# Kernel optimization log

Hardware: AMD Instinct MI355X
Metric: run time of the kernel (lower is better)

The kernel has to match this reference:

```python
import jax, jax.numpy as jnp
import numpy as np

N = 131072
IN_A = 256
IN_V = 512
IN_VF = 512
CH = 256
BN_EPS = 1e-5
COS_EPS = 1e-8


def setup_inputs() -> dict:
    key = jax.random.key(0)
    ks = jax.random.split(key, 12)
    s = 0.05
    return {
        "x": jax.random.normal(ks[0], (N, 4, 512), dtype=jnp.float32),
        "audio_node_mask": jax.random.bernoulli(ks[1], 0.5, (N,)),
        "W_a": jax.random.normal(ks[2], (IN_A, CH), dtype=jnp.float32) * s,
        "b_a": jnp.zeros((CH,), jnp.float32),
        "W_v": jax.random.normal(ks[3], (IN_V, CH), dtype=jnp.float32) * s,
        "b_v": jnp.zeros((CH,), jnp.float32),
        "W_f": jax.random.normal(ks[4], (2 * CH, CH), dtype=jnp.float32) * s,
        "b_f": jnp.zeros((CH,), jnp.float32),
        "gamma": jnp.ones((CH,), jnp.float32),
        "beta": jnp.zeros((CH,), jnp.float32),
        "W_fc": jax.random.normal(ks[5], (CH, 2), dtype=jnp.float32) * s,
        "b_fc": jnp.zeros((2,), jnp.float32),
    }


def reference(x, audio_node_mask, W_a, b_a, W_v, b_v, W_f, b_f, gamma, beta, W_fc, b_fc):
    # Slice per-type features (x: [N, 4, 512])
    a_in = x[:, 0, :IN_A]    # audio feats (also video->audio feats)
    v_in = x[:, 1, :IN_V]    # video feats
    a_vf = x[:, 2, :IN_VF]   # audio voice-face emb
    v_vf = x[:, 3, :IN_VF]   # video voice-face emb

    # cosine similarity along feature dim (torch.nn.functional.cosine_similarity semantics)
    dot = jnp.sum(a_vf * v_vf, axis=1)
    denom = jnp.maximum(jnp.linalg.norm(a_vf, axis=1) * jnp.linalg.norm(v_vf, axis=1), COS_EPS)
    sim = dot / denom  # [N]

    # per-type linears (compute densely, select by mask -> same math as masked scatter)
    a_out = a_in @ W_a + b_a                                   # [N, CH]
    v_out = v_in @ W_v + b_v                                   # [N, CH]
    va = a_in * sim[:, None]                                   # sim-weighted audio feats on video nodes
    fused = jnp.concatenate([va, v_out], axis=1) @ W_f + b_f   # [N, CH]

    graph_feats = jnp.where(audio_node_mask[:, None], a_out, fused)

    # BatchNorm1d (training: batch statistics, biased variance)
    mu = jnp.mean(graph_feats, axis=0)
    var = jnp.mean(jnp.square(graph_feats - mu), axis=0)
    graph_feats = (graph_feats - mu) * jax.lax.rsqrt(var + BN_EPS) * gamma + beta

    graph_feats = jax.nn.relu(graph_feats)
    return graph_feats @ W_fc + b_fc  # [N, 2]
```

## Files before the change

kernel.cpp:

```cpp
#include <hip/hip_runtime.h>
#include <hip/hip_bf16.h>
#include <stdint.h>

#define NN 131072
#define NB2 2050

typedef unsigned int uint;
typedef unsigned short ushort;
typedef __attribute__((ext_vector_type(8))) __bf16 bf16x8;
typedef __attribute__((ext_vector_type(2))) __bf16 bf16x2;
typedef __attribute__((ext_vector_type(4))) float f32x4;


__device__ __forceinline__ ushort f2bf(float f) {
    uint u = __float_as_uint(f);
    u += 0x7FFF + ((u >> 16) & 1);
    return (ushort)(u >> 16);
}
__device__ __forceinline__ uint pk2(float a, float b) {
    bf16x2 t;
    t[0] = (__bf16)a;
    t[1] = (__bf16)b;
    return __builtin_bit_cast(uint, t);
}
__device__ __forceinline__ bool mask_val(const unsigned char* m8, int flag, int i) {
    return flag ? (m8[(size_t)i * 4] != 0) : (m8[i] != 0);
}
__device__ __forceinline__ size_t pack_off(int k, int c) {
    return (size_t)(((k >> 5) * 16 + (c >> 4)) * 512
                    + (((k >> 3) & 3) * 16 + (c & 15)) * 8 + (k & 7));
}

__global__ void k_detect(const uint4* m128, int n, int* cntNZ) {
    __shared__ int cnt;
    if (threadIdx.x == 0) cnt = 0;
    __syncthreads();
    int local = 0;
    int nv = n >> 4;
    #pragma unroll 4
    for (int i = threadIdx.x; i < nv; i += 1024) {
        uint4 v = m128[i];
        if ((v.x | v.y | v.z | v.w) & 0x0000FF00u) local = 1;
    }
    if (local) atomicAdd(&cnt, 1);
    __syncthreads();
    if (threadIdx.x == 0) *cntNZ = cnt;
}

__global__ void k_count(const unsigned char* m8, const int* cntNZp, int* cntM) {
    int flag = (*cntNZp == 0) ? 1 : 0;
    int t = threadIdx.x;
    bool m = mask_val(m8, flag, blockIdx.x * 256 + t);
    unsigned long long bal = __ballot(m);
    __shared__ int wsum[4];
    if ((t & 63) == 0) wsum[t >> 6] = __popcll(bal);
    __syncthreads();
    if (t == 0) cntM[blockIdx.x] = wsum[0] + wsum[1] + wsum[2] + wsum[3];
}

__global__ void k_scan(const int* __restrict__ cntM, int* __restrict__ meta,
                       int* __restrict__ baseA, int* __restrict__ baseF) {
    __shared__ int sA[512], sF[512];
    int t = threadIdx.x;
    int a = cntM[t], f = 256 - a;
    sA[t] = a; sF[t] = f;
    __syncthreads();
    for (int off = 1; off < 512; off <<= 1) {
        int va = (t >= off) ? sA[t - off] : 0;
        int vf = (t >= off) ? sF[t - off] : 0;
        __syncthreads();
        sA[t] += va; sF[t] += vf;
        __syncthreads();
    }
    baseA[t] = sA[t] - a;
    baseF[t] = sF[t] - f;
    if (t == 511) { meta[2] = sA[511]; meta[1] = sF[511]; }
}

__global__ void k_fill(const unsigned char* m8, const int* cntNZp,
                       const int* __restrict__ baseA, const int* __restrict__ baseF,
                       int* __restrict__ audioIdx, int* __restrict__ fusedIdx) {
    int flag = (*cntNZp == 0) ? 1 : 0;
    int blk = blockIdx.x, t = threadIdx.x;
    int row = blk * 256 + t;
    bool m = mask_val(m8, flag, row);
    unsigned long long bal = __ballot(m);
    int lane = t & 63, w = t >> 6;
    unsigned long long lt = (1ull << lane) - 1ull;
    int pA = __popcll(bal & lt);
    __shared__ int wA[4];
    if (lane == 0) wA[w] = __popcll(bal);
    __syncthreads();
    int offA = 0;
    for (int i = 0; i < w; ++i) offA += wA[i];
    int offF = w * 64 - offA;
    int pF = lane - pA;
    if (m) audioIdx[baseA[blk] + offA + pA] = row;
    else   fusedIdx[baseF[blk] + offF + pF] = row;
}

__global__ void k_prep(const float* __restrict__ Wa, const float* __restrict__ Wf,
                       const float* __restrict__ Wv, const float* __restrict__ bv,
                       const float* __restrict__ bf_, ushort* __restrict__ Bwa,
                       ushort* __restrict__ Bwf, float* __restrict__ cf) {
    int c = threadIdx.x;
    int b = blockIdx.x;
    if (b < 256) {
        Bwa[pack_off(b, c)] = f2bf(Wa[b * 256 + c]);
    } else if (b < 512) {
        Bwf[pack_off(512 + (b - 256), c)] = f2bf(Wf[(b - 256) * 256 + c]);
    } else if (b < 1024) {
        int k = b - 512;
        const float* wr = Wv + k * 256;
        float acc = 0.f;
        #pragma unroll 8
        for (int j = 0; j < 256; ++j) acc += wr[j] * Wf[(256 + j) * 256 + c];
        Bwf[pack_off(k, c)] = f2bf(acc);
    } else {
        float acc = bf_[c];
        #pragma unroll 8
        for (int j = 0; j < 256; ++j) acc += bv[j] * Wf[(256 + j) * 256 + c];
        cf[c] = acc;
    }
}

__global__ __launch_bounds__(512, 4) void k_main(
    const float* __restrict__ x, const int* __restrict__ meta,
    const int* __restrict__ fusedIdx, const int* __restrict__ audioIdx,
    const ushort* __restrict__ Bwa, const ushort* __restrict__ Bwf,
    const float* __restrict__ ba, const float* __restrict__ cf,
    ushort* __restrict__ gf, float* __restrict__ bn_s, float* __restrict__ bn_q)
{
    __shared__ ushort As[2][64 * 256];
    __shared__ int ridxS[64];
    __shared__ float simS[64];
    __shared__ unsigned char validS[64];
    __shared__ float redS[256], redQ[256];

    const int tid = threadIdx.x;
    const int cntF = meta[1], cntA = meta[2];
    const int nbF = (cntF + 63) >> 6;
    const int nbA = (cntA + 63) >> 6;
    const int b = blockIdx.x;
    const bool isF = b < nbF;
    const int bb = isF ? b : b - nbF;

    if (!isF && bb >= nbA) {
        if (tid < 256) {
            bn_s[(size_t)b * 256 + tid] = 0.f;
            bn_q[(size_t)b * 256 + tid] = 0.f;
        }
        return;
    }

    const int cnt = isF ? cntF : cntA;
    const int* idxArr = isF ? fusedIdx : audioIdx;
    const int lane = tid & 63;
    const int w = tid >> 6, wr = w >> 2, wc = w & 3;
    const int fr = lane & 15, fg = lane >> 4;

    if (tid < 64) {
        int gpos = bb * 64 + tid;
        int ok = gpos < cnt;
        ridxS[tid] = ok ? idxArr[gpos] : 0;
        validS[tid] = ok;
        simS[tid] = 1.f;
    }
    if (tid < 256) { redS[tid] = 0.f; redQ[tid] = 0.f; }
    __syncthreads();

    const int sr2 = tid >> 3, kq = tid & 7;
    const float* xrow = x + (size_t)ridxS[sr2] * 2048;
    const float sVf = validS[sr2] ? 1.f : 0.f;

    f32x4 t0_, t1_, t2_, t3_, t4_, t5_, t6_, t7_;
    auto loadV = [&](int baseF_) {
        const f32x4* src = (const f32x4*)(xrow + baseF_) + kq * 8;
        t0_ = src[0]; t1_ = src[1]; t2_ = src[2]; t3_ = src[3];
        t4_ = src[4]; t5_ = src[5]; t6_ = src[6]; t7_ = src[7];
    };
    auto storeV = [&](int buf, float scl) {
        ushort* dst = As[buf] + sr2 * 256;
        int sx = sr2 & 7;
        uint4 q;
        q.x = pk2(t0_.x * scl, t0_.y * scl); q.y = pk2(t0_.z * scl, t0_.w * scl);
        q.z = pk2(t1_.x * scl, t1_.y * scl); q.w = pk2(t1_.z * scl, t1_.w * scl);
        *(uint4*)(dst + (((kq * 4 + 0) ^ sx) << 3)) = q;
        q.x = pk2(t2_.x * scl, t2_.y * scl); q.y = pk2(t2_.z * scl, t2_.w * scl);
        q.z = pk2(t3_.x * scl, t3_.y * scl); q.w = pk2(t3_.z * scl, t3_.w * scl);
        *(uint4*)(dst + (((kq * 4 + 1) ^ sx) << 3)) = q;
        q.x = pk2(t4_.x * scl, t4_.y * scl); q.y = pk2(t4_.z * scl, t4_.w * scl);
        q.z = pk2(t5_.x * scl, t5_.y * scl); q.w = pk2(t5_.z * scl, t5_.w * scl);
        *(uint4*)(dst + (((kq * 4 + 2) ^ sx) << 3)) = q;
        q.x = pk2(t6_.x * scl, t6_.y * scl); q.y = pk2(t6_.z * scl, t6_.w * scl);
        q.z = pk2(t7_.x * scl, t7_.y * scl); q.w = pk2(t7_.z * scl, t7_.w * scl);
        *(uint4*)(dst + (((kq * 4 + 3) ^ sx) << 3)) = q;
    };

    const ushort* bBase = (isF ? Bwf : Bwa) + ((size_t)(wc * 4) << 9) + (lane << 3);
    const int r0 = wr * 32 + fr, r1 = r0 + 16;
    const ushort* prd0 = As[0] + r0 * 256;
    const int sx0 = r0 & 7, sx1 = r1 & 7;

    f32x4 acc[2][4];
    #pragma unroll
    for (int m = 0; m < 2; ++m)
        #pragma unroll
        for (int n = 0; n < 4; ++n) acc[m][n] = (f32x4){0.f, 0.f, 0.f, 0.f};

    auto compute4 = [&](int buf, int visit) {
        const ushort* p0 = As[buf] + r0 * 256;
        const ushort* p1 = As[buf] + r1 * 256;
        #pragma unroll
        for (int st = 0; st < 4; ++st) {
            #pragma unroll
            for (int kk = 0; kk < 2; ++kk) {
                int sl = st * 8 + kk * 4 + fg;
                bf16x8 a0 = *(const bf16x8*)(p0 + ((sl ^ sx0) << 3));
                bf16x8 a1 = *(const bf16x8*)(p1 + ((sl ^ sx1) << 3));
                int kb = (visit * 4 + st) * 2 + kk;
                #pragma unroll
                for (int n = 0; n < 4; ++n) {
                    bf16x8 bv = *(const bf16x8*)(bBase + ((size_t)(kb * 16 + n) << 9));
                    acc[0][n] = __builtin_amdgcn_mfma_f32_16x16x32_bf16(a0, bv, acc[0][n], 0, 0, 0);
                    acc[1][n] = __builtin_amdgcn_mfma_f32_16x16x32_bf16(a1, bv, acc[1][n], 0, 0, 0);
                }
            }
        }
    };

    if (isF) {
        loadV(512);
        #pragma unroll 2
        for (int rr = 0; rr < 8; ++rr) {
            int r = w * 8 + rr;
            const f32x4* p = (const f32x4*)(x + (size_t)ridxS[r] * 2048 + 1024);
            f32x4 a0 = p[lane], a1 = p[lane + 64];
            f32x4 v0 = p[lane + 128], v1 = p[lane + 192];
            float dot = a0.x * v0.x + a0.y * v0.y + a0.z * v0.z + a0.w * v0.w
                      + a1.x * v1.x + a1.y * v1.y + a1.z * v1.z + a1.w * v1.w;
            float na = a0.x * a0.x + a0.y * a0.y + a0.z * a0.z + a0.w * a0.w
                     + a1.x * a1.x + a1.y * a1.y + a1.z * a1.z + a1.w * a1.w;
            float nv = v0.x * v0.x + v0.y * v0.y + v0.z * v0.z + v0.w * v0.w
                     + v1.x * v1.x + v1.y * v1.y + v1.z * v1.z + v1.w * v1.w;
            #pragma unroll
            for (int off = 32; off; off >>= 1) {
                dot += __shfl_xor(dot, off);
                na  += __shfl_xor(na,  off);
                nv  += __shfl_xor(nv,  off);
            }
            if (lane == 0)
                simS[r] = dot / fmaxf(sqrtf(na * nv), 1e-8f);
        }
        storeV(0, sVf);
        loadV(768);
        __syncthreads();
        compute4(0, 0);
        storeV(1, sVf);
        float sAf = validS[sr2] ? simS[sr2] : 0.f;
        __syncthreads();
        loadV(0);
        compute4(1, 1);
        storeV(0, sAf);
        __syncthreads();
        compute4(0, 2);
    } else {
        loadV(0);
        storeV(0, sVf);
        __syncthreads();
        compute4(0, 0);
    }

    const int colLo = wc * 64 + fr;
    const float* biasp = isF ? cf : ba;
    float bN[4];
    #pragma unroll
    for (int n = 0; n < 4; ++n) bN[n] = biasp[colLo + n * 16];

    float cs[4] = {0.f, 0.f, 0.f, 0.f}, cq[4] = {0.f, 0.f, 0.f, 0.f};
    #pragma unroll
    for (int m = 0; m < 2; ++m) {
        #pragma unroll
        for (int j = 0; j < 4; ++j) {
            int rloc = wr * 32 + m * 16 + fg * 4 + j;
            if (validS[rloc]) {
                ushort* grow = gf + (size_t)ridxS[rloc] * 256;
                #pragma unroll
                for (int n = 0; n < 4; ++n) {
                    float g = acc[m][n][j] + bN[n];
                    grow[colLo + n * 16] = f2bf(g);
                    cs[n] += g;
                    cq[n] += g * g;
                }
            }
        }
    }
    #pragma unroll
    for (int n = 0; n < 4; ++n) {
        atomicAdd(&redS[colLo + n * 16], cs[n]);
        atomicAdd(&redQ[colLo + n * 16], cq[n]);
    }
    __syncthreads();
    if (tid < 256) {
        bn_s[(size_t)b * 256 + tid] = redS[tid];
        bn_q[(size_t)b * 256 + tid] = redQ[tid];
    }
}

__global__ void k_stats(const float* __restrict__ bn_s, const float* __restrict__ bn_q,
                        const float* __restrict__ gamma, const float* __restrict__ beta,
                        float* __restrict__ scale, float* __restrict__ shift) {
    int c = blockIdx.x;
    int t = threadIdx.x;
    float s = 0.f, q = 0.f;
    for (int r = t; r < NB2; r += 256) {
        s += bn_s[(size_t)r * 256 + c];
        q += bn_q[(size_t)r * 256 + c];
    }
    __shared__ float ss[256], qq[256];
    ss[t] = s; qq[t] = q;
    __syncthreads();
    for (int off = 128; off; off >>= 1) {
        if (t < off) { ss[t] += ss[t + off]; qq[t] += qq[t + off]; }
        __syncthreads();
    }
    if (t == 0) {
        float mu  = ss[0] / 131072.f;
        float var = qq[0] / 131072.f - mu * mu;
        float sc = gamma[c] * rsqrtf(var + 1e-5f);
        scale[c] = sc;
        shift[c] = beta[c] - mu * sc;
    }
}

__global__ void k_out(const ushort* __restrict__ gf, const float* __restrict__ scale,
                      const float* __restrict__ shift, const float* __restrict__ Wfc,
                      const float* __restrict__ bfc, float* __restrict__ out) {
    int wid = threadIdx.x >> 6;
    int lane = threadIdx.x & 63;
    int hl = lane & 31;
    int i = blockIdx.x * 8 + wid * 2 + (lane >> 5);
    uint4 gv = ((const uint4*)(gf + (size_t)i * 256))[hl];
    int c0 = hl * 8;
    float g[8];
    g[0] = __uint_as_float(gv.x << 16); g[1] = __uint_as_float(gv.x & 0xFFFF0000u);
    g[2] = __uint_as_float(gv.y << 16); g[3] = __uint_as_float(gv.y & 0xFFFF0000u);
    g[4] = __uint_as_float(gv.z << 16); g[5] = __uint_as_float(gv.z & 0xFFFF0000u);
    g[6] = __uint_as_float(gv.w << 16); g[7] = __uint_as_float(gv.w & 0xFFFF0000u);
    float p0 = 0.f, p1 = 0.f;
    #pragma unroll
    for (int j = 0; j < 2; ++j) {
        f32x4 sc = *(const f32x4*)(scale + c0 + j * 4);
        f32x4 sh = *(const f32x4*)(shift + c0 + j * 4);
        f32x4 w0 = *(const f32x4*)(Wfc + (c0 + j * 4) * 2);
        f32x4 w1 = *(const f32x4*)(Wfc + (c0 + j * 4) * 2 + 4);
        float y0 = fmaxf(g[j * 4 + 0] * sc.x + sh.x, 0.f);
        float y1 = fmaxf(g[j * 4 + 1] * sc.y + sh.y, 0.f);
        float y2 = fmaxf(g[j * 4 + 2] * sc.z + sh.z, 0.f);
        float y3 = fmaxf(g[j * 4 + 3] * sc.w + sh.w, 0.f);
        p0 += y0 * w0.x + y1 * w0.z + y2 * w1.x + y3 * w1.z;
        p1 += y0 * w0.y + y1 * w0.w + y2 * w1.y + y3 * w1.w;
    }
    #pragma unroll
    for (int off = 16; off; off >>= 1) {
        p0 += __shfl_xor(p0, off);
        p1 += __shfl_xor(p1, off);
    }
    if (hl == 0) {
        out[(size_t)i * 2]     = p0 + bfc[0];
        out[(size_t)i * 2 + 1] = p1 + bfc[1];
    }
}

extern "C" void kernel_launch(void* const* d_in, const int* in_sizes, int n_in,
                              void* d_out, int out_size, void* d_ws, size_t ws_size,
                              hipStream_t stream) {
    const float* x          = (const float*)d_in[0];
    const unsigned char* mk = (const unsigned char*)d_in[1];
    const float* Wa  = (const float*)d_in[2];
    const float* ba  = (const float*)d_in[3];
    const float* Wv  = (const float*)d_in[4];
    const float* bv  = (const float*)d_in[5];
    const float* Wf  = (const float*)d_in[6];
    const float* bf  = (const float*)d_in[7];
    const float* gamma = (const float*)d_in[8];
    const float* beta  = (const float*)d_in[9];
    const float* Wfc = (const float*)d_in[10];
    const float* bfc = (const float*)d_in[11];
    float* out = (float*)d_out;

    char* ws = (char*)d_ws;
    int*    meta   = (int*)ws;
    float*  scale  = (float*)(ws + 1024);
    float*  shift  = (float*)(ws + 2048);
    float*  cf     = (float*)(ws + 3072);
    int*    cntM   = (int*)(ws + 8192);
    int*    baseA  = (int*)(ws + 12288);
    int*    baseF  = (int*)(ws + 16384);
    ushort* Bwa    = (ushort*)(ws + 32768);
    ushort* Bwf    = (ushort*)(ws + 262144);
    int*    fusedIdx = (int*)(ws + (1u << 20));
    int*    audioIdx = (int*)(ws + (1u << 20) + (512u << 10));
    float*  bn_s   = (float*)(ws + (8u << 20));
    float*  bn_q   = (float*)(ws + (16u << 20));
    ushort* gf     = (ushort*)(ws + (32u << 20));

    int n = in_sizes[1];

    k_detect<<<1, 1024, 0, stream>>>((const uint4*)mk, n, meta);
    k_count<<<512, 256, 0, stream>>>(mk, meta, cntM);
    k_scan<<<1, 512, 0, stream>>>(cntM, meta, baseA, baseF);
    k_fill<<<512, 256, 0, stream>>>(mk, meta, baseA, baseF, audioIdx, fusedIdx);
    k_prep<<<1025, 256, 0, stream>>>(Wa, Wf, Wv, bv, bf, Bwa, Bwf, cf);
    k_main<<<NB2, 512, 0, stream>>>(x, meta, fusedIdx, audioIdx, Bwa, Bwf, ba, cf,
                                    gf, bn_s, bn_q);
    k_stats<<<256, 256, 0, stream>>>(bn_s, bn_q, gamma, beta, scale, shift);
    k_out<<<NN / 8, 256, 0, stream>>>(gf, scale, shift, Wfc, bfc, out);
}
```

Measured before the change: 254.2 us.

## Restructure main GEMM so each wave owns 16 rows across all columns without LDS

The main kernel no longer stages the gathered activations in shared memory with double buffering. Each wave now loads its own 16 rows straight from global memory into MFMA A-fragments and computes all 256 output columns with 16 accumulators. Blocks cover 128 rows instead of 64, which halves the grid, and the per-column BN partial sums are first reduced with wave shuffles before the shared atomics. This removes LDS traffic and block barriers, but it raises register pressure (16 accumulator tiles) and makes each wave read the full weight matrix from global or cache, so weight traffic per row grows.

Result: slower. 295.0 us (+16.1%).

```diff
diff --git a/kernel.cpp b/kernel.cpp
--- a/kernel.cpp
+++ b/kernel.cpp
@@ -3,7 +3,7 @@
 #include <stdint.h>
 
 #define NN 131072
-#define NB2 2050
+#define NB_MAIN 1025
 
 typedef unsigned int uint;
 typedef unsigned short ushort;
@@ -131,16 +131,12 @@
     const float* __restrict__ ba, const float* __restrict__ cf,
     ushort* __restrict__ gf, float* __restrict__ bn_s, float* __restrict__ bn_q)
 {
-    __shared__ ushort As[2][64 * 256];
-    __shared__ int ridxS[64];
-    __shared__ float simS[64];
-    __shared__ unsigned char validS[64];
     __shared__ float redS[256], redQ[256];
 
     const int tid = threadIdx.x;
     const int cntF = meta[1], cntA = meta[2];
-    const int nbF = (cntF + 63) >> 6;
-    const int nbA = (cntA + 63) >> 6;
+    const int nbF = (cntF + 127) >> 7;
+    const int nbA = (cntA + 127) >> 7;
     const int b = blockIdx.x;
     const bool isF = b < nbF;
     const int bb = isF ? b : b - nbF;
@@ -156,85 +152,24 @@
     const int cnt = isF ? cntF : cntA;
     const int* idxArr = isF ? fusedIdx : audioIdx;
     const int lane = tid & 63;
-    const int w = tid >> 6, wr = w >> 2, wc = w & 3;
+    const int w = tid >> 6;
     const int fr = lane & 15, fg = lane >> 4;
 
-    if (tid < 64) {
-        int gpos = bb * 64 + tid;
-        int ok = gpos < cnt;
-        ridxS[tid] = ok ? idxArr[gpos] : 0;
-        validS[tid] = ok;
-        simS[tid] = 1.f;
-    }
     if (tid < 256) { redS[tid] = 0.f; redQ[tid] = 0.f; }
     __syncthreads();
 
-    const int sr2 = tid >> 3, kq = tid & 7;
-    const float* xrow = x + (size_t)ridxS[sr2] * 2048;
-    const float sVf = validS[sr2] ? 1.f : 0.f;
-
-    f32x4 t0_, t1_, t2_, t3_, t4_, t5_, t6_, t7_;
-    auto loadV = [&](int baseF_) {
-        const f32x4* src = (const f32x4*)(xrow + baseF_) + kq * 8;
-        t0_ = src[0]; t1_ = src[1]; t2_ = src[2]; t3_ = src[3];
-        t4_ = src[4]; t5_ = src[5]; t6_ = src[6]; t7_ = src[7];
-    };
-    auto storeV = [&](int buf, float scl) {
-        ushort* dst = As[buf] + sr2 * 256;
-        int sx = sr2 & 7;
-        uint4 q;
-        q.x = pk2(t0_.x * scl, t0_.y * scl); q.y = pk2(t0_.z * scl, t0_.w * scl);
-        q.z = pk2(t1_.x * scl, t1_.y * scl); q.w = pk2(t1_.z * scl, t1_.w * scl);
-        *(uint4*)(dst + (((kq * 4 + 0) ^ sx) << 3)) = q;
-        q.x = pk2(t2_.x * scl, t2_.y * scl); q.y = pk2(t2_.z * scl, t2_.w * scl);
-        q.z = pk2(t3_.x * scl, t3_.y * scl); q.w = pk2(t3_.z * scl, t3_.w * scl);
-        *(uint4*)(dst + (((kq * 4 + 1) ^ sx) << 3)) = q;
-        q.x = pk2(t4_.x * scl, t4_.y * scl); q.y = pk2(t4_.z * scl, t4_.w * scl);
-        q.z = pk2(t5_.x * scl, t5_.y * scl); q.w = pk2(t5_.z * scl, t5_.w * scl);
-        *(uint4*)(dst + (((kq * 4 + 2) ^ sx) << 3)) = q;
-        q.x = pk2(t6_.x * scl, t6_.y * scl); q.y = pk2(t6_.z * scl, t6_.w * scl);
-        q.z = pk2(t7_.x * scl, t7_.y * scl); q.w = pk2(t7_.z * scl, t7_.w * scl);
-        *(uint4*)(dst + (((kq * 4 + 3) ^ sx) << 3)) = q;
-    };
-
-    const ushort* bBase = (isF ? Bwf : Bwa) + ((size_t)(wc * 4) << 9) + (lane << 3);
-    const int r0 = wr * 32 + fr, r1 = r0 + 16;
-    const ushort* prd0 = As[0] + r0 * 256;
-    const int sx0 = r0 & 7, sx1 = r1 & 7;
-
-    f32x4 acc[2][4];
-    #pragma unroll
-    for (int m = 0; m < 2; ++m)
-        #pragma unroll
-        for (int n = 0; n < 4; ++n) acc[m][n] = (f32x4){0.f, 0.f, 0.f, 0.f};
-
-    auto compute4 = [&](int buf, int visit) {
-        const ushort* p0 = As[buf] + r0 * 256;
-        const ushort* p1 = As[buf] + r1 * 256;
-        #pragma unroll
-        for (int st = 0; st < 4; ++st) {
-            #pragma unroll
-            for (int kk = 0; kk < 2; ++kk) {
-                int sl = st * 8 + kk * 4 + fg;
-                bf16x8 a0 = *(const bf16x8*)(p0 + ((sl ^ sx0) << 3));
-                bf16x8 a1 = *(const bf16x8*)(p1 + ((sl ^ sx1) << 3));
-                int kb = (visit * 4 + st) * 2 + kk;
-                #pragma unroll
-                for (int n = 0; n < 4; ++n) {
-                    bf16x8 bv = *(const bf16x8*)(bBase + ((size_t)(kb * 16 + n) << 9));
-                    acc[0][n] = __builtin_amdgcn_mfma_f32_16x16x32_bf16(a0, bv, acc[0][n], 0, 0, 0);
-                    acc[1][n] = __builtin_amdgcn_mfma_f32_16x16x32_bf16(a1, bv, acc[1][n], 0, 0, 0);
-                }
-            }
-        }
-    };
+    const int gpos = bb * 128 + w * 16 + fr;
+    const bool valid = gpos < cnt;
+    const int ridx = valid ? idxArr[gpos] : 0;
+    const float sv = valid ? 1.f : 0.f;
+    const float* xrow = x + (size_t)ridx * 2048;
+    float simv = 1.f;
 
     if (isF) {
-        loadV(512);
         #pragma unroll 2
-        for (int rr = 0; rr < 8; ++rr) {
-            int r = w * 8 + rr;
-            const f32x4* p = (const f32x4*)(x + (size_t)ridxS[r] * 2048 + 1024);
+        for (int rr = 0; rr < 16; ++rr) {
+            int rowi = __shfl(ridx, rr);
+            const f32x4* p = (const f32x4*)(x + (size_t)rowi * 2048 + 1024);
             f32x4 a0 = p[lane], a1 = p[lane + 64];
             f32x4 v0 = p[lane + 128], v1 = p[lane + 192];
             float dot = a0.x * v0.x + a0.y * v0.y + a0.z * v0.z + a0.w * v0.w
@@ -249,56 +184,77 @@
                 na  += __shfl_xor(na,  off);
                 nv  += __shfl_xor(nv,  off);
             }
-            if (lane == 0)
-                simS[r] = dot / fmaxf(sqrtf(na * nv), 1e-8f);
-        }
-        storeV(0, sVf);
-        loadV(768);
-        __syncthreads();
-        compute4(0, 0);
-        storeV(1, sVf);
-        float sAf = validS[sr2] ? simS[sr2] : 0.f;
-        __syncthreads();
-        loadV(0);
-        compute4(1, 1);
-        storeV(0, sAf);
-        __syncthreads();
-        compute4(0, 2);
-    } else {
-        loadV(0);
-        storeV(0, sVf);
-        __syncthreads();
-        compute4(0, 0);
-    }
-
-    const int colLo = wc * 64 + fr;
+            float s = dot / fmaxf(sqrtf(na * nv), 1e-8f);
+            if (rr == fr) simv = s;
+        }
+    }
+    const float sSim = simv * sv;
+
+    const int NS = isF ? 24 : 8;
+    const ushort* bB = (isF ? Bwf : Bwa) + (lane << 3);
+
+    f32x4 acc[16];
+    #pragma unroll
+    for (int n = 0; n < 16; ++n) acc[n] = (f32x4){0.f, 0.f, 0.f, 0.f};
+
+    #pragma unroll 4
+    for (int st = 0; st < NS; ++st) {
+        const int koff = isF ? ((st < 16) ? 512 + st * 32 : (st - 16) * 32)
+                             : st * 32;
+        const float scl = (isF && st >= 16) ? sSim : sv;
+        const f32x4* ap = (const f32x4*)(xrow + koff) + fg * 2;
+        f32x4 u0 = ap[0], u1 = ap[1];
+        int4 q;
+        q.x = pk2(u0.x * scl, u0.y * scl);
+        q.y = pk2(u0.z * scl, u0.w * scl);
+        q.z = pk2(u1.x * scl, u1.y * scl);
+        q.w = pk2(u1.z * scl, u1.w * scl);
+        bf16x8 af = __builtin_bit_cast(bf16x8, q);
+        #pragma unroll
+        for (int n = 0; n < 16; ++n) {
+            bf16x8 bv = *(const bf16x8*)(bB + ((size_t)(st * 16 + n) << 9));
+            acc[n] = __builtin_amdgcn_mfma_f32_16x16x32_bf16(af, bv, acc[n], 0, 0, 0);
+        }
+    }
+
     const float* biasp = isF ? cf : ba;
-    float bN[4];
-    #pragma unroll
-    for (int n = 0; n < 4; ++n) bN[n] = biasp[colLo + n * 16];
-
-    float cs[4] = {0.f, 0.f, 0.f, 0.f}, cq[4] = {0.f, 0.f, 0.f, 0.f};
-    #pragma unroll
-    for (int m = 0; m < 2; ++m) {
+    float bN[16];
+    #pragma unroll
+    for (int n = 0; n < 16; ++n) bN[n] = biasp[n * 16 + fr];
+
+    float cs[16], cq[16];
+    #pragma unroll
+    for (int n = 0; n < 16; ++n) { cs[n] = 0.f; cq[n] = 0.f; }
+
+    #pragma unroll
+    for (int j = 0; j < 4; ++j) {
+        int rloc = fg * 4 + j;
+        bool vj = (bb * 128 + w * 16 + rloc) < cnt;
+        int rj = __shfl(ridx, rloc);
+        ushort* grow = gf + (size_t)rj * 256;
         #pragma unroll
-        for (int j = 0; j < 4; ++j) {
-            int rloc = wr * 32 + m * 16 + fg * 4 + j;
-            if (validS[rloc]) {
-                ushort* grow = gf + (size_t)ridxS[rloc] * 256;
-                #pragma unroll
-                for (int n = 0; n < 4; ++n) {
-                    float g = acc[m][n][j] + bN[n];
-                    grow[colLo + n * 16] = f2bf(g);
-                    cs[n] += g;
-                    cq[n] += g * g;
-                }
+        for (int n = 0; n < 16; ++n) {
+            float g = acc[n][j] + bN[n];
+            if (vj) {
+                grow[n * 16 + fr] = f2bf(g);
+                cs[n] += g;
+                cq[n] += g * g;
             }
         }
     }
     #pragma unroll
-    for (int n = 0; n < 4; ++n) {
-        atomicAdd(&redS[colLo + n * 16], cs[n]);
-        atomicAdd(&redQ[colLo + n * 16], cq[n]);
+    for (int n = 0; n < 16; ++n) {
+        cs[n] += __shfl_xor(cs[n], 16);
+        cs[n] += __shfl_xor(cs[n], 32);
+        cq[n] += __shfl_xor(cq[n], 16);
+        cq[n] += __shfl_xor(cq[n], 32);
+    }
+    if (fg == 0) {
+        #pragma unroll
+        for (int n = 0; n < 16; ++n) {
+            atomicAdd(&redS[n * 16 + fr], cs[n]);
+            atomicAdd(&redQ[n * 16 + fr], cq[n]);
+        }
     }
     __syncthreads();
     if (tid < 256) {
@@ -313,7 +269,7 @@
     int c = blockIdx.x;
     int t = threadIdx.x;
     float s = 0.f, q = 0.f;
-    for (int r = t; r < NB2; r += 256) {
+    for (int r = t; r < NB_MAIN; r += 256) {
         s += bn_s[(size_t)r * 256 + c];
         q += bn_q[(size_t)r * 256 + c];
     }
@@ -412,8 +368,8 @@
     k_scan<<<1, 512, 0, stream>>>(cntM, meta, baseA, baseF);
     k_fill<<<512, 256, 0, stream>>>(mk, meta, baseA, baseF, audioIdx, fusedIdx);
     k_prep<<<1025, 256, 0, stream>>>(Wa, Wf, Wv, bv, bf, Bwa, Bwf, cf);
-    k_main<<<NB2, 512, 0, stream>>>(x, meta, fusedIdx, audioIdx, Bwa, Bwf, ba, cf,
-                                    gf, bn_s, bn_q);
+    k_main<<<NB_MAIN, 512, 0, stream>>>(x, meta, fusedIdx, audioIdx, Bwa, Bwf, ba, cf,
+                                        gf, bn_s, bn_q);
     k_stats<<<256, 256, 0, stream>>>(bn_s, bn_q, gamma, beta, scale, shift);
     k_out<<<NN / 8, 256, 0, stream>>>(gf, scale, shift, Wfc, bfc, out);
 }
```
